# Kernel optimization log

Hardware: AMD Instinct MI355X
Metric: run time of the kernel (lower is better)

The kernel has to match this reference:

```python
import jax, jax.numpy as jnp
import numpy as np

# AdEx constants (match init_kwargs)
THR = -50.4
EL = -70.6
GL = 30.0
C = 281.0
DELTAT = 2.0
V_RESET = -70.6
TAUW = 144.0
A = 4.0
B = 0.0805
DT = 1.0
N_REFRAC = 5
DAMP = 0.3
DT_GL__C = DT * GL / C
DT_A__TAUW = DT * A / TAUW

BATCH, N_IN, UNITS = 8192, 256, 1024


@jax.custom_vjp
def spike_function(v_scaled):
    return (v_scaled > 0.0).astype(jnp.float32)

def _spike_fwd(v_scaled):
    return spike_function(v_scaled), v_scaled

def _spike_bwd(v_scaled, dy):
    # pseudo-derivative: dampening * max(1 - |v_scaled|, 0)
    return (dy * DAMP * jnp.maximum(1.0 - jnp.abs(v_scaled), 0.0),)

spike_function.defvjp(_spike_fwd, _spike_bwd)


def setup_inputs() -> dict:
    key = jax.random.key(0)
    ks = jax.random.split(key, 7)
    inputs = jax.random.normal(ks[0], (BATCH, N_IN), dtype=jnp.float32)
    old_v = EL + 5.0 * jax.random.normal(ks[1], (BATCH, UNITS), dtype=jnp.float32)
    old_r = jax.random.randint(ks[2], (BATCH, UNITS), 0, N_REFRAC, dtype=jnp.int32)
    old_w = jax.random.normal(ks[3], (BATCH, UNITS), dtype=jnp.float32)
    old_z = (jax.random.uniform(ks[4], (BATCH, UNITS)) < 0.1).astype(jnp.float32)
    input_weights = jax.random.uniform(ks[5], (N_IN, UNITS), dtype=jnp.float32, minval=0.0, maxval=1.2)
    recurrent_weights = 0.7 * jax.random.normal(ks[6], (UNITS, UNITS), dtype=jnp.float32) / np.sqrt(UNITS)
    return {"inputs": inputs, "old_v": old_v, "old_r": old_r, "old_w": old_w,
            "old_z": old_z, "input_weights": input_weights,
            "recurrent_weights": recurrent_weights}


def reference(inputs, old_v, old_r, old_w, old_z, input_weights, recurrent_weights):
    units = recurrent_weights.shape[0]
    disconnect = jnp.eye(units, dtype=bool)  # no autapses on diagonal
    no_autapse_w_rec = jnp.where(disconnect, 0.0, recurrent_weights)

    i_t = inputs @ input_weights + old_z @ no_autapse_w_rec  # (B, U)

    exp_terms = jnp.clip(jnp.exp((old_v - THR) / DELTAT), -1e6, 30.0 / DT_GL__C)
    exp_terms = jax.lax.stop_gradient(exp_terms)

    new_v = (old_v - DT_GL__C * (old_v - EL)
             + DT_GL__C * DELTAT * exp_terms
             + (i_t - old_w) * DT / C)
    new_v = jnp.where(old_z > 0.5, V_RESET, new_v)

    new_w = old_w - DT / TAUW * old_w + DT_A__TAUW * (old_v - EL) + B * old_z

    is_refractory = old_r > 0
    v_scaled = -(THR - new_v) / (THR - EL)
    new_z = spike_function(v_scaled)
    new_z = jnp.where(is_refractory, 0.0, new_z)

    new_r = jnp.clip(old_r - 1 + (new_z * N_REFRAC).astype(jnp.int32), 0, N_REFRAC)

    return new_v, new_z, new_r, new_w
```

## Files before the change

kernel.cpp:

```cpp
#include <hip/hip_runtime.h>
#include <stdint.h>

#define THRC      (-50.4f)
#define ELC       (-70.6f)
#define V_RESETC  (-70.6f)
#define DT_GL_C   (0.10676156583629893f)
#define DELTATC   (2.0f)
#define DT_C      (0.0035587188612099642f)
#define DT_TAUW   (0.006944444444444444f)
#define DTA_TAUW  (0.027777777777777776f)
#define BCONST    (0.0805f)
#define EXPCLIP   (281.0f)

#define M_TOT 8192
#define N_IN  256
#define UNITS 1024
#define K_TOT 1792
#define CH    (8192*1024)

typedef __attribute__((ext_vector_type(8))) short s16x8;
typedef __attribute__((ext_vector_type(4))) float f32x4;

__device__ __forceinline__ unsigned short f2bf(float f) {
  union { float f; unsigned int u; } v; v.f = f;
  unsigned int r = v.u + 0x7fffu + ((v.u >> 16) & 1u);
  return (unsigned short)(r >> 16);
}
__device__ __forceinline__ float bf2f(unsigned short h) {
  union { unsigned int u; float f; } v; v.u = ((unsigned int)h) << 16; return v.f;
}

__device__ __forceinline__ void gload_lds16(const void* g, void* l) {
  __builtin_amdgcn_global_load_lds(
      (const __attribute__((address_space(1))) void*)g,
      (__attribute__((address_space(3))) void*)l, 16, 0, 0);
}

__global__ __launch_bounds__(256) void build_a(const float* __restrict__ X,
                                               const float* __restrict__ Z,
                                               unsigned short* __restrict__ A) {
  int o = blockIdx.x * 256 + threadIdx.x;
  int row = o / 224;
  int c8 = (o - row * 224) * 8;
  const float* src; bool lo = false;
  if (c8 < 256)        { src = X + (size_t)row * 256 + c8; }
  else if (c8 < 512)   { src = X + (size_t)row * 256 + (c8 - 256); lo = true; }
  else if (c8 < 768)   { src = X + (size_t)row * 256 + (c8 - 512); }
  else                 { src = Z + (size_t)row * 1024 + (c8 - 768); }
  float4 f0 = *(const float4*)(src);
  float4 f1 = *(const float4*)(src + 4);
  float fv[8] = {f0.x, f0.y, f0.z, f0.w, f1.x, f1.y, f1.z, f1.w};
  unsigned short h[8];
#pragma unroll
  for (int i = 0; i < 8; ++i) {
    unsigned short hi = f2bf(fv[i]);
    h[i] = lo ? f2bf(fv[i] - bf2f(hi)) : hi;
  }
  uint4 pk;
  pk.x = (unsigned)h[0] | ((unsigned)h[1] << 16);
  pk.y = (unsigned)h[2] | ((unsigned)h[3] << 16);
  pk.z = (unsigned)h[4] | ((unsigned)h[5] << 16);
  pk.w = (unsigned)h[6] | ((unsigned)h[7] << 16);
  *(uint4*)(A + (size_t)row * K_TOT + c8) = pk;
}

__global__ __launch_bounds__(256) void build_b(const float* __restrict__ Wi,
                                               const float* __restrict__ Wr,
                                               unsigned short* __restrict__ BT) {
  __shared__ unsigned short tile[32][33];
  int tx = threadIdx.x & 31, ty = threadIdx.x >> 5;
  int k0 = blockIdx.x * 32, n0 = blockIdx.y * 32;
#pragma unroll
  for (int j = 0; j < 4; ++j) {
    int kk = k0 + ty + j * 8;
    int n  = n0 + tx;
    float f; bool lo = false;
    if (kk < 256)       f = Wi[(size_t)kk * 1024 + n];
    else if (kk < 512)  f = Wi[(size_t)(kk - 256) * 1024 + n];
    else if (kk < 768) { f = Wi[(size_t)(kk - 512) * 1024 + n]; lo = true; }
    else { int kr = kk - 768; f = (kr == n) ? 0.0f : Wr[(size_t)kr * 1024 + n]; }
    unsigned short h = f2bf(f);
    if (lo) h = f2bf(f - bf2f(h));
    tile[ty + j * 8][tx] = h;
  }
  __syncthreads();
#pragma unroll
  for (int j = 0; j < 4; ++j) {
    int n  = n0 + ty + j * 8;
    int kk = k0 + tx;
    BT[(size_t)n * K_TOT + kk] = tile[tx][ty + j * 8];
  }
}

__global__ __launch_bounds__(256) void adex_gemm(
    const unsigned short* __restrict__ A, const unsigned short* __restrict__ BT,
    const float* __restrict__ oV, const int* __restrict__ oR,
    const float* __restrict__ oW, const float* __restrict__ oZ,
    float* __restrict__ out)
{
  __shared__ unsigned short As[128 * 32];
  __shared__ unsigned short Bs[128 * 32];
  const int tid  = threadIdx.x;
  const int wid  = tid >> 6;
  const int lane = tid & 63;
  const int rowA0 = blockIdx.x * 128;
  const int colB0 = blockIdx.y * 128;

  f32x4 acc[4][4];
#pragma unroll
  for (int i = 0; i < 4; ++i)
#pragma unroll
    for (int j = 0; j < 4; ++j) acc[i][j] = (f32x4){0.f, 0.f, 0.f, 0.f};

  const int ar = tid >> 2;
  const int ac = (tid & 3) * 8;
  const unsigned short* aSrc0 = A  + (size_t)(rowA0 + ar)      * K_TOT + ac;
  const unsigned short* aSrc1 = A  + (size_t)(rowA0 + 64 + ar) * K_TOT + ac;
  const unsigned short* bSrc0 = BT + (size_t)(colB0 + ar)      * K_TOT + ac;
  const unsigned short* bSrc1 = BT + (size_t)(colB0 + 64 + ar) * K_TOT + ac;
  unsigned short* aDst0 = As + tid * 8;
  unsigned short* aDst1 = As + 2048 + tid * 8;
  unsigned short* bDst0 = Bs + tid * 8;
  unsigned short* bDst1 = Bs + 2048 + tid * 8;

  const int wr  = (wid >> 1) * 64, wc = (wid & 1) * 64;
  const int l15 = lane & 15, l4 = lane >> 4;

  for (int ks = 0; ks < K_TOT / 32; ++ks) {
    gload_lds16(aSrc0, aDst0);
    gload_lds16(aSrc1, aDst1);
    gload_lds16(bSrc0, bDst0);
    gload_lds16(bSrc1, bDst1);
    aSrc0 += 32; aSrc1 += 32; bSrc0 += 32; bSrc1 += 32;
    asm volatile("s_waitcnt vmcnt(0)" ::: "memory");
    __syncthreads();

    s16x8 af[4], bfv[4];
#pragma unroll
    for (int f = 0; f < 4; ++f)
      af[f] = *(const s16x8*)(As + (wr + f * 16 + l15) * 32 + l4 * 8);
#pragma unroll
    for (int f = 0; f < 4; ++f)
      bfv[f] = *(const s16x8*)(Bs + (wc + f * 16 + l15) * 32 + l4 * 8);
#pragma unroll
    for (int i = 0; i < 4; ++i)
#pragma unroll
      for (int j = 0; j < 4; ++j)
        acc[i][j] = __builtin_amdgcn_mfma_f32_16x16x32_bf16(af[i], bfv[j], acc[i][j], 0, 0, 0);
    __syncthreads();
  }

#pragma unroll
  for (int i = 0; i < 4; ++i) {
    int mBase = rowA0 + wr + i * 16 + l4 * 4;
#pragma unroll
    for (int j = 0; j < 4; ++j) {
      int u = colB0 + wc + j * 16 + l15;
#pragma unroll
      for (int r = 0; r < 4; ++r) {
        int m = mBase + r;
        size_t idx = (size_t)m * UNITS + u;
        float it = acc[i][j][r];
        float ov = oV[idx];
        float ow = oW[idx];
        float oz = oZ[idx];
        int   orr = oR[idx];
        float ex = expf((ov - THRC) * 0.5f);
        ex = fminf(ex, EXPCLIP);
        float nv = ov - DT_GL_C * (ov - ELC) + (DT_GL_C * DELTATC) * ex + (it - ow) * DT_C;
        nv = (oz > 0.5f) ? V_RESETC : nv;
        float nw = ow - DT_TAUW * ow + DTA_TAUW * (ov - ELC) + BCONST * oz;
        float nz = (nv > THRC) ? 1.0f : 0.0f;
        if (orr > 0) nz = 0.0f;
        int nr = orr - 1 + (nz > 0.5f ? 5 : 0);
        nr = nr < 0 ? 0 : (nr > 5 ? 5 : nr);
        out[idx]           = nv;
        out[CH + idx]      = nz;
        out[2 * CH + idx]  = (float)nr;
        out[3 * CH + idx]  = nw;
      }
    }
  }
}

extern "C" void kernel_launch(void* const* d_in, const int* in_sizes, int n_in,
                              void* d_out, int out_size, void* d_ws, size_t ws_size,
                              hipStream_t stream) {
  const float* X  = (const float*)d_in[0];
  const float* oV = (const float*)d_in[1];
  const int*   oR = (const int*)d_in[2];
  const float* oW = (const float*)d_in[3];
  const float* oZ = (const float*)d_in[4];
  const float* Wi = (const float*)d_in[5];
  const float* Wr = (const float*)d_in[6];
  unsigned short* Aall = (unsigned short*)d_ws;
  unsigned short* BT   = Aall + (size_t)M_TOT * K_TOT;
  float* out = (float*)d_out;

  hipLaunchKernelGGL(build_a, dim3((M_TOT * (K_TOT / 8)) / 256), dim3(256), 0, stream, X, oZ, Aall);
  hipLaunchKernelGGL(build_b, dim3(K_TOT / 32, UNITS / 32), dim3(256), 0, stream, Wi, Wr, BT);
  hipLaunchKernelGGL(adex_gemm, dim3(M_TOT / 128, UNITS / 128), dim3(256), 0, stream,
                     Aall, BT, oV, oR, oW, oZ, out);
}
```

Baseline: 120.9 us.

## Double-buffer LDS tiles, swizzle K layout, and shrink GEMM tile to 128x64

Adds two LDS buffers so global-to-LDS loads for the next K step are issued while MFMAs run on the current one. Workspace A/B rows get an XOR swizzle of their 8-element K slots, and the reads apply the same swizzle to avoid LDS bank conflicts. The tile shrinks from 128x128 to 128x64 on a 1D grid that walks M first, doubling the block count and lowering per-block register and LDS use (launch bounds ask for 4 blocks per CU). The cost is less reuse per block and more total global traffic for A.

After: 146.9 us. 1.21x slower.

```diff
diff --git a/kernel.cpp b/kernel.cpp
--- a/kernel.cpp
+++ b/kernel.cpp
@@ -13,10 +13,12 @@
 #define EXPCLIP   (281.0f)
 
 #define M_TOT 8192
-#define N_IN  256
 #define UNITS 1024
 #define K_TOT 1792
 #define CH    (8192*1024)
+#define BM 128
+#define BN 64
+#define NKSTEPS (K_TOT/32)
 
 typedef __attribute__((ext_vector_type(8))) short s16x8;
 typedef __attribute__((ext_vector_type(4))) float f32x4;
@@ -34,6 +36,10 @@
   __builtin_amdgcn_global_load_lds(
       (const __attribute__((address_space(1))) void*)g,
       (__attribute__((address_space(3))) void*)l, 16, 0, 0);
+}
+
+__device__ __forceinline__ int swz_col(int row, int k) {
+  return (k & ~31) | (((((k >> 3) & 3) ^ ((row >> 1) & 3)) << 3)) | (k & 7);
 }
 
 __global__ __launch_bounds__(256) void build_a(const float* __restrict__ X,
@@ -61,7 +67,7 @@
   pk.y = (unsigned)h[2] | ((unsigned)h[3] << 16);
   pk.z = (unsigned)h[4] | ((unsigned)h[5] << 16);
   pk.w = (unsigned)h[6] | ((unsigned)h[7] << 16);
-  *(uint4*)(A + (size_t)row * K_TOT + c8) = pk;
+  *(uint4*)(A + (size_t)row * K_TOT + swz_col(row, c8)) = pk;
 }
 
 __global__ __launch_bounds__(256) void build_b(const float* __restrict__ Wi,
@@ -88,73 +94,84 @@
   for (int j = 0; j < 4; ++j) {
     int n  = n0 + ty + j * 8;
     int kk = k0 + tx;
-    BT[(size_t)n * K_TOT + kk] = tile[tx][ty + j * 8];
-  }
-}
-
-__global__ __launch_bounds__(256) void adex_gemm(
+    BT[(size_t)n * K_TOT + swz_col(n, kk)] = tile[tx][ty + j * 8];
+  }
+}
+
+__global__ __launch_bounds__(256, 4) void adex_gemm(
     const unsigned short* __restrict__ A, const unsigned short* __restrict__ BT,
     const float* __restrict__ oV, const int* __restrict__ oR,
     const float* __restrict__ oW, const float* __restrict__ oZ,
     float* __restrict__ out)
 {
-  __shared__ unsigned short As[128 * 32];
-  __shared__ unsigned short Bs[128 * 32];
+  __shared__ unsigned short As[2][BM * 32];
+  __shared__ unsigned short Bs[2][BN * 32];
   const int tid  = threadIdx.x;
   const int wid  = tid >> 6;
   const int lane = tid & 63;
-  const int rowA0 = blockIdx.x * 128;
-  const int colB0 = blockIdx.y * 128;
-
-  f32x4 acc[4][4];
+  const int mt = blockIdx.x & 63;
+  const int nt = blockIdx.x >> 6;
+  const int rowA0 = mt * BM;
+  const int colB0 = nt * BN;
+
+  f32x4 acc[4][2];
 #pragma unroll
   for (int i = 0; i < 4; ++i)
 #pragma unroll
-    for (int j = 0; j < 4; ++j) acc[i][j] = (f32x4){0.f, 0.f, 0.f, 0.f};
-
-  const int ar = tid >> 2;
-  const int ac = (tid & 3) * 8;
-  const unsigned short* aSrc0 = A  + (size_t)(rowA0 + ar)      * K_TOT + ac;
-  const unsigned short* aSrc1 = A  + (size_t)(rowA0 + 64 + ar) * K_TOT + ac;
-  const unsigned short* bSrc0 = BT + (size_t)(colB0 + ar)      * K_TOT + ac;
-  const unsigned short* bSrc1 = BT + (size_t)(colB0 + 64 + ar) * K_TOT + ac;
-  unsigned short* aDst0 = As + tid * 8;
-  unsigned short* aDst1 = As + 2048 + tid * 8;
-  unsigned short* bDst0 = Bs + tid * 8;
-  unsigned short* bDst1 = Bs + 2048 + tid * 8;
-
-  const int wr  = (wid >> 1) * 64, wc = (wid & 1) * 64;
+    for (int j = 0; j < 2; ++j) acc[i][j] = (f32x4){0.f, 0.f, 0.f, 0.f};
+
+  const int srow = tid >> 2, sslot = tid & 3;
+  const unsigned short* aS0 = A  + (size_t)(rowA0 + srow) * K_TOT + sslot * 8;
+  const unsigned short* aS1 = aS0 + (size_t)64 * K_TOT;
+  const unsigned short* bS  = BT + (size_t)(colB0 + srow) * K_TOT + sslot * 8;
+
   const int l15 = lane & 15, l4 = lane >> 4;
-
-  for (int ks = 0; ks < K_TOT / 32; ++ks) {
-    gload_lds16(aSrc0, aDst0);
-    gload_lds16(aSrc1, aDst1);
-    gload_lds16(bSrc0, bDst0);
-    gload_lds16(bSrc1, bDst1);
-    aSrc0 += 32; aSrc1 += 32; bSrc0 += 32; bSrc1 += 32;
+  const int wr = (wid >> 1) * 64, wc = (wid & 1) * 32;
+  const int slot = l4 ^ ((l15 >> 1) & 3);
+  int offA[4], offB[2];
+#pragma unroll
+  for (int f = 0; f < 4; ++f) offA[f] = (wr + f * 16 + l15) * 32 + slot * 8;
+#pragma unroll
+  for (int f = 0; f < 2; ++f) offB[f] = (wc + f * 16 + l15) * 32 + slot * 8;
+
+#define STAGE(buf)                                            \
+  do {                                                        \
+    gload_lds16(aS0, &As[buf][0] + tid * 8);                  \
+    gload_lds16(aS1, &As[buf][0] + 2048 + tid * 8);           \
+    gload_lds16(bS,  &Bs[buf][0] + tid * 8);                  \
+    aS0 += 32; aS1 += 32; bS += 32;                           \
+  } while (0)
+
+  STAGE(0);
+  asm volatile("s_waitcnt vmcnt(0)" ::: "memory");
+  __syncthreads();
+
+  int cur = 0;
+  for (int ks = 0; ks < NKSTEPS; ++ks) {
+    if (ks + 1 < NKSTEPS) STAGE(cur ^ 1);
+    const unsigned short* ab = &As[cur][0];
+    const unsigned short* bb = &Bs[cur][0];
+    s16x8 af[4], bfv[2];
+#pragma unroll
+    for (int f = 0; f < 4; ++f) af[f]  = *(const s16x8*)(ab + offA[f]);
+#pragma unroll
+    for (int f = 0; f < 2; ++f) bfv[f] = *(const s16x8*)(bb + offB[f]);
+#pragma unroll
+    for (int i = 0; i < 4; ++i)
+#pragma unroll
+      for (int j = 0; j < 2; ++j)
+        acc[i][j] = __builtin_amdgcn_mfma_f32_16x16x32_bf16(af[i], bfv[j], acc[i][j], 0, 0, 0);
     asm volatile("s_waitcnt vmcnt(0)" ::: "memory");
     __syncthreads();
-
-    s16x8 af[4], bfv[4];
-#pragma unroll
-    for (int f = 0; f < 4; ++f)
-      af[f] = *(const s16x8*)(As + (wr + f * 16 + l15) * 32 + l4 * 8);
-#pragma unroll
-    for (int f = 0; f < 4; ++f)
-      bfv[f] = *(const s16x8*)(Bs + (wc + f * 16 + l15) * 32 + l4 * 8);
-#pragma unroll
-    for (int i = 0; i < 4; ++i)
-#pragma unroll
-      for (int j = 0; j < 4; ++j)
-        acc[i][j] = __builtin_amdgcn_mfma_f32_16x16x32_bf16(af[i], bfv[j], acc[i][j], 0, 0, 0);
-    __syncthreads();
-  }
+    cur ^= 1;
+  }
+#undef STAGE
 
 #pragma unroll
   for (int i = 0; i < 4; ++i) {
     int mBase = rowA0 + wr + i * 16 + l4 * 4;
 #pragma unroll
-    for (int j = 0; j < 4; ++j) {
+    for (int j = 0; j < 2; ++j) {
       int u = colB0 + wc + j * 16 + l15;
 #pragma unroll
       for (int r = 0; r < 4; ++r) {
@@ -199,6 +216,6 @@
 
   hipLaunchKernelGGL(build_a, dim3((M_TOT * (K_TOT / 8)) / 256), dim3(256), 0, stream, X, oZ, Aall);
   hipLaunchKernelGGL(build_b, dim3(K_TOT / 32, UNITS / 32), dim3(256), 0, stream, Wi, Wr, BT);
-  hipLaunchKernelGGL(adex_gemm, dim3(M_TOT / 128, UNITS / 128), dim3(256), 0, stream,
+  hipLaunchKernelGGL(adex_gemm, dim3((M_TOT / BM) * (UNITS / BN)), dim3(256), 0, stream,
                      Aall, BT, oV, oR, oW, oZ, out);
 }
```

## Replace LDS-staged GEMM with single-wave blocks loading fragments directly from global

Applied to the files above, without the earlier changes.

The GEMM now launches one 64-thread wave per 64x64 output tile. Each wave loads its MFMA operand fragments straight from global memory, so the LDS staging buffers and both per-step barriers are gone. Block indices are swizzled so that neighbouring blocks share A and B tiles in cache. This removes LDS round-trips and barrier stalls, but it gives up operand sharing across waves, which raises L2 traffic. Loads are also unpipelined and issued as strided 16-byte row segments.

Result: slower. 211.0 us (+74.4%).

```diff
diff --git a/kernel.cpp b/kernel.cpp
--- a/kernel.cpp
+++ b/kernel.cpp
@@ -13,10 +13,10 @@
 #define EXPCLIP   (281.0f)
 
 #define M_TOT 8192
-#define N_IN  256
 #define UNITS 1024
 #define K_TOT 1792
 #define CH    (8192*1024)
+#define NKSTEPS (K_TOT/32)
 
 typedef __attribute__((ext_vector_type(8))) short s16x8;
 typedef __attribute__((ext_vector_type(4))) float f32x4;
@@ -28,12 +28,6 @@
 }
 __device__ __forceinline__ float bf2f(unsigned short h) {
   union { unsigned int u; float f; } v; v.u = ((unsigned int)h) << 16; return v.f;
-}
-
-__device__ __forceinline__ void gload_lds16(const void* g, void* l) {
-  __builtin_amdgcn_global_load_lds(
-      (const __attribute__((address_space(1))) void*)g,
-      (__attribute__((address_space(3))) void*)l, 16, 0, 0);
 }
 
 __global__ __launch_bounds__(256) void build_a(const float* __restrict__ X,
@@ -92,19 +86,30 @@
   }
 }
 
-__global__ __launch_bounds__(256) void adex_gemm(
+__global__ __launch_bounds__(64) void adex_gemm(
     const unsigned short* __restrict__ A, const unsigned short* __restrict__ BT,
     const float* __restrict__ oV, const int* __restrict__ oR,
     const float* __restrict__ oW, const float* __restrict__ oZ,
     float* __restrict__ out)
 {
-  __shared__ unsigned short As[128 * 32];
-  __shared__ unsigned short Bs[128 * 32];
-  const int tid  = threadIdx.x;
-  const int wid  = tid >> 6;
-  const int lane = tid & 63;
-  const int rowA0 = blockIdx.x * 128;
-  const int colB0 = blockIdx.y * 128;
+  const int lane = threadIdx.x;
+  const int l15 = lane & 15, l4 = lane >> 4;
+
+  const int bid = blockIdx.x;
+  const int swz = (bid & 7) * 256 + (bid >> 3);
+  const int nt = swz & 15;
+  const int mt = swz >> 4;
+  const int rowA0 = mt * 64;
+  const int colB0 = nt * 64;
+
+  const unsigned short* pA0 = A  + (size_t)(rowA0 +  0 + l15) * K_TOT + l4 * 8;
+  const unsigned short* pA1 = A  + (size_t)(rowA0 + 16 + l15) * K_TOT + l4 * 8;
+  const unsigned short* pA2 = A  + (size_t)(rowA0 + 32 + l15) * K_TOT + l4 * 8;
+  const unsigned short* pA3 = A  + (size_t)(rowA0 + 48 + l15) * K_TOT + l4 * 8;
+  const unsigned short* pB0 = BT + (size_t)(colB0 +  0 + l15) * K_TOT + l4 * 8;
+  const unsigned short* pB1 = BT + (size_t)(colB0 + 16 + l15) * K_TOT + l4 * 8;
+  const unsigned short* pB2 = BT + (size_t)(colB0 + 32 + l15) * K_TOT + l4 * 8;
+  const unsigned short* pB3 = BT + (size_t)(colB0 + 48 + l15) * K_TOT + l4 * 8;
 
   f32x4 acc[4][4];
 #pragma unroll
@@ -112,50 +117,31 @@
 #pragma unroll
     for (int j = 0; j < 4; ++j) acc[i][j] = (f32x4){0.f, 0.f, 0.f, 0.f};
 
-  const int ar = tid >> 2;
-  const int ac = (tid & 3) * 8;
-  const unsigned short* aSrc0 = A  + (size_t)(rowA0 + ar)      * K_TOT + ac;
-  const unsigned short* aSrc1 = A  + (size_t)(rowA0 + 64 + ar) * K_TOT + ac;
-  const unsigned short* bSrc0 = BT + (size_t)(colB0 + ar)      * K_TOT + ac;
-  const unsigned short* bSrc1 = BT + (size_t)(colB0 + 64 + ar) * K_TOT + ac;
-  unsigned short* aDst0 = As + tid * 8;
-  unsigned short* aDst1 = As + 2048 + tid * 8;
-  unsigned short* bDst0 = Bs + tid * 8;
-  unsigned short* bDst1 = Bs + 2048 + tid * 8;
-
-  const int wr  = (wid >> 1) * 64, wc = (wid & 1) * 64;
-  const int l15 = lane & 15, l4 = lane >> 4;
-
-  for (int ks = 0; ks < K_TOT / 32; ++ks) {
-    gload_lds16(aSrc0, aDst0);
-    gload_lds16(aSrc1, aDst1);
-    gload_lds16(bSrc0, bDst0);
-    gload_lds16(bSrc1, bDst1);
-    aSrc0 += 32; aSrc1 += 32; bSrc0 += 32; bSrc1 += 32;
-    asm volatile("s_waitcnt vmcnt(0)" ::: "memory");
-    __syncthreads();
-
-    s16x8 af[4], bfv[4];
 #pragma unroll
-    for (int f = 0; f < 4; ++f)
-      af[f] = *(const s16x8*)(As + (wr + f * 16 + l15) * 32 + l4 * 8);
-#pragma unroll
-    for (int f = 0; f < 4; ++f)
-      bfv[f] = *(const s16x8*)(Bs + (wc + f * 16 + l15) * 32 + l4 * 8);
+  for (int s = 0; s < NKSTEPS; ++s) {
+    const int o = s * 32;
+    s16x8 af[4], bf[4];
+    af[0] = *(const s16x8*)(pA0 + o);
+    af[1] = *(const s16x8*)(pA1 + o);
+    af[2] = *(const s16x8*)(pA2 + o);
+    af[3] = *(const s16x8*)(pA3 + o);
+    bf[0] = *(const s16x8*)(pB0 + o);
+    bf[1] = *(const s16x8*)(pB1 + o);
+    bf[2] = *(const s16x8*)(pB2 + o);
+    bf[3] = *(const s16x8*)(pB3 + o);
 #pragma unroll
     for (int i = 0; i < 4; ++i)
 #pragma unroll
       for (int j = 0; j < 4; ++j)
-        acc[i][j] = __builtin_amdgcn_mfma_f32_16x16x32_bf16(af[i], bfv[j], acc[i][j], 0, 0, 0);
-    __syncthreads();
+        acc[i][j] = __builtin_amdgcn_mfma_f32_16x16x32_bf16(af[i], bf[j], acc[i][j], 0, 0, 0);
   }
 
 #pragma unroll
   for (int i = 0; i < 4; ++i) {
-    int mBase = rowA0 + wr + i * 16 + l4 * 4;
+    int mBase = rowA0 + i * 16 + l4 * 4;
 #pragma unroll
     for (int j = 0; j < 4; ++j) {
-      int u = colB0 + wc + j * 16 + l15;
+      int u = colB0 + j * 16 + l15;
 #pragma unroll
       for (int r = 0; r < 4; ++r) {
         int m = mBase + r;
@@ -199,6 +185,6 @@
 
   hipLaunchKernelGGL(build_a, dim3((M_TOT * (K_TOT / 8)) / 256), dim3(256), 0, stream, X, oZ, Aall);
   hipLaunchKernelGGL(build_b, dim3(K_TOT / 32, UNITS / 32), dim3(256), 0, stream, Wi, Wr, BT);
-  hipLaunchKernelGGL(adex_gemm, dim3(M_TOT / 128, UNITS / 128), dim3(256), 0, stream,
+  hipLaunchKernelGGL(adex_gemm, dim3((M_TOT / 64) * (UNITS / 64)), dim3(64), 0, stream,
                      Aall, BT, oV, oR, oW, oZ, out);
 }
```

## Restructure GEMM: tall 512x32 tiles, A from global, double-buffered B in LDS

Applied to the files above, without the earlier changes.

The GEMM kernel now uses 512-thread blocks computing 512x32 output tiles. Each wave reads its A fragments straight from global memory into registers, and only the B panel is staged in LDS, double-buffered over 256-wide K super-steps with a single barrier per super-step. A block-index swizzle groups blocks so that nearby blocks share A and B tiles in cache. The trade-off is that A is re-read from global by every N-tile (32 column tiles) with no LDS reuse, and the per-wave tile shrinks to 64x32, which lowers MFMA work per loaded byte.

Result: slower. 203.6 us (+68.3%).

```diff
diff --git a/kernel.cpp b/kernel.cpp
--- a/kernel.cpp
+++ b/kernel.cpp
@@ -13,10 +13,14 @@
 #define EXPCLIP   (281.0f)
 
 #define M_TOT 8192
-#define N_IN  256
 #define UNITS 1024
 #define K_TOT 1792
 #define CH    (8192*1024)
+#define BM 512
+#define BN 32
+#define SK 256
+#define NSUP (K_TOT / SK)
+#define KSPS (SK / 32)
 
 typedef __attribute__((ext_vector_type(8))) short s16x8;
 typedef __attribute__((ext_vector_type(4))) float f32x4;
@@ -92,70 +96,80 @@
   }
 }
 
-__global__ __launch_bounds__(256) void adex_gemm(
+__global__ __launch_bounds__(512, 4) void adex_gemm(
     const unsigned short* __restrict__ A, const unsigned short* __restrict__ BT,
     const float* __restrict__ oV, const int* __restrict__ oR,
     const float* __restrict__ oW, const float* __restrict__ oZ,
     float* __restrict__ out)
 {
-  __shared__ unsigned short As[128 * 32];
-  __shared__ unsigned short Bs[128 * 32];
+  __shared__ unsigned short Bs[2][32][32][8];
   const int tid  = threadIdx.x;
-  const int wid  = tid >> 6;
+  const int w    = tid >> 6;
   const int lane = tid & 63;
-  const int rowA0 = blockIdx.x * 128;
-  const int colB0 = blockIdx.y * 128;
-
-  f32x4 acc[4][4];
+  const int l15  = lane & 15, l4 = lane >> 4;
+
+  const int bid = blockIdx.x;
+  const int swz = (bid & 7) * 64 + (bid >> 3);
+  const int mt    = swz >> 5;
+  const int ntile = swz & 31;
+  const int rowA0 = mt * BM;
+  const int colB0 = ntile * BN;
+
+  const int u0 = tid, u1 = tid + 512;
+  const unsigned short* bSrc0 = BT + (size_t)(colB0 + (u0 & 31)) * K_TOT + (u0 >> 5) * 8;
+  const unsigned short* bSrc1 = BT + (size_t)(colB0 + (u1 & 31)) * K_TOT + (u1 >> 5) * 8;
+
+#define STAGE_B(buf, k0)                                                      \
+  do {                                                                        \
+    gload_lds16(bSrc0 + (k0), (unsigned short*)Bs[buf] + w * 512);            \
+    gload_lds16(bSrc1 + (k0), (unsigned short*)Bs[buf] + 4096 + w * 512);     \
+  } while (0)
+
+  const unsigned short* pA0 = A + (size_t)(rowA0 + w * 64 +  0 + l15) * K_TOT + l4 * 8;
+  const unsigned short* pA1 = A + (size_t)(rowA0 + w * 64 + 16 + l15) * K_TOT + l4 * 8;
+  const unsigned short* pA2 = A + (size_t)(rowA0 + w * 64 + 32 + l15) * K_TOT + l4 * 8;
+  const unsigned short* pA3 = A + (size_t)(rowA0 + w * 64 + 48 + l15) * K_TOT + l4 * 8;
+
+  f32x4 acc[4][2];
 #pragma unroll
   for (int i = 0; i < 4; ++i)
 #pragma unroll
-    for (int j = 0; j < 4; ++j) acc[i][j] = (f32x4){0.f, 0.f, 0.f, 0.f};
-
-  const int ar = tid >> 2;
-  const int ac = (tid & 3) * 8;
-  const unsigned short* aSrc0 = A  + (size_t)(rowA0 + ar)      * K_TOT + ac;
-  const unsigned short* aSrc1 = A  + (size_t)(rowA0 + 64 + ar) * K_TOT + ac;
-  const unsigned short* bSrc0 = BT + (size_t)(colB0 + ar)      * K_TOT + ac;
-  const unsigned short* bSrc1 = BT + (size_t)(colB0 + 64 + ar) * K_TOT + ac;
-  unsigned short* aDst0 = As + tid * 8;
-  unsigned short* aDst1 = As + 2048 + tid * 8;
-  unsigned short* bDst0 = Bs + tid * 8;
-  unsigned short* bDst1 = Bs + 2048 + tid * 8;
-
-  const int wr  = (wid >> 1) * 64, wc = (wid & 1) * 64;
-  const int l15 = lane & 15, l4 = lane >> 4;
-
-  for (int ks = 0; ks < K_TOT / 32; ++ks) {
-    gload_lds16(aSrc0, aDst0);
-    gload_lds16(aSrc1, aDst1);
-    gload_lds16(bSrc0, bDst0);
-    gload_lds16(bSrc1, bDst1);
-    aSrc0 += 32; aSrc1 += 32; bSrc0 += 32; bSrc1 += 32;
-    asm volatile("s_waitcnt vmcnt(0)" ::: "memory");
+    for (int j = 0; j < 2; ++j) acc[i][j] = (f32x4){0.f, 0.f, 0.f, 0.f};
+
+  STAGE_B(0, 0);
+  __syncthreads();
+
+  for (int sup = 0; sup < NSUP; ++sup) {
+    const int buf = sup & 1;
+    if (sup + 1 < NSUP) STAGE_B(buf ^ 1, (sup + 1) * SK);
+#pragma unroll
+    for (int ks = 0; ks < KSPS; ++ks) {
+      s16x8 af0 = *(const s16x8*)(pA0 + ks * 32);
+      s16x8 af1 = *(const s16x8*)(pA1 + ks * 32);
+      s16x8 af2 = *(const s16x8*)(pA2 + ks * 32);
+      s16x8 af3 = *(const s16x8*)(pA3 + ks * 32);
+      s16x8 bf0 = *(const s16x8*)(&Bs[buf][ks * 4 + l4][l15][0]);
+      s16x8 bf1 = *(const s16x8*)(&Bs[buf][ks * 4 + l4][16 + l15][0]);
+      acc[0][0] = __builtin_amdgcn_mfma_f32_16x16x32_bf16(af0, bf0, acc[0][0], 0, 0, 0);
+      acc[0][1] = __builtin_amdgcn_mfma_f32_16x16x32_bf16(af0, bf1, acc[0][1], 0, 0, 0);
+      acc[1][0] = __builtin_amdgcn_mfma_f32_16x16x32_bf16(af1, bf0, acc[1][0], 0, 0, 0);
+      acc[1][1] = __builtin_amdgcn_mfma_f32_16x16x32_bf16(af1, bf1, acc[1][1], 0, 0, 0);
+      acc[2][0] = __builtin_amdgcn_mfma_f32_16x16x32_bf16(af2, bf0, acc[2][0], 0, 0, 0);
+      acc[2][1] = __builtin_amdgcn_mfma_f32_16x16x32_bf16(af2, bf1, acc[2][1], 0, 0, 0);
+      acc[3][0] = __builtin_amdgcn_mfma_f32_16x16x32_bf16(af3, bf0, acc[3][0], 0, 0, 0);
+      acc[3][1] = __builtin_amdgcn_mfma_f32_16x16x32_bf16(af3, bf1, acc[3][1], 0, 0, 0);
+    }
+    pA0 += SK; pA1 += SK; pA2 += SK; pA3 += SK;
     __syncthreads();
-
-    s16x8 af[4], bfv[4];
-#pragma unroll
-    for (int f = 0; f < 4; ++f)
-      af[f] = *(const s16x8*)(As + (wr + f * 16 + l15) * 32 + l4 * 8);
-#pragma unroll
-    for (int f = 0; f < 4; ++f)
-      bfv[f] = *(const s16x8*)(Bs + (wc + f * 16 + l15) * 32 + l4 * 8);
-#pragma unroll
-    for (int i = 0; i < 4; ++i)
-#pragma unroll
-      for (int j = 0; j < 4; ++j)
-        acc[i][j] = __builtin_amdgcn_mfma_f32_16x16x32_bf16(af[i], bfv[j], acc[i][j], 0, 0, 0);
-    __syncthreads();
-  }
+  }
+#undef STAGE_B
 
 #pragma unroll
   for (int i = 0; i < 4; ++i) {
-    int mBase = rowA0 + wr + i * 16 + l4 * 4;
-#pragma unroll
-    for (int j = 0; j < 4; ++j) {
-      int u = colB0 + wc + j * 16 + l15;
+    int mBase = rowA0 + w * 64 + i * 16 + l4 * 4;
+#pragma unroll
+    for (int j = 0; j < 2; ++j) {
+      int u = colB0 + j * 16 + l15;
 #pragma unroll
       for (int r = 0; r < 4; ++r) {
         int m = mBase + r;
@@ -199,6 +213,6 @@
 
   hipLaunchKernelGGL(build_a, dim3((M_TOT * (K_TOT / 8)) / 256), dim3(256), 0, stream, X, oZ, Aall);
   hipLaunchKernelGGL(build_b, dim3(K_TOT / 32, UNITS / 32), dim3(256), 0, stream, Wi, Wr, BT);
-  hipLaunchKernelGGL(adex_gemm, dim3(M_TOT / 128, UNITS / 128), dim3(256), 0, stream,
+  hipLaunchKernelGGL(adex_gemm, dim3((M_TOT / BM) * (UNITS / BN)), dim3(512), 0, stream,
                      Aall, BT, oV, oR, oW, oZ, out);
 }
```
